# Kernel optimization log

Hardware: AMD Instinct MI355X
Metric: run time of the kernel (lower is better)

Reference implementation:

```python
import jax, jax.numpy as jnp
import numpy as np

NEG_SLOPE = 0.2  # PyG GATConv default negative_slope
N_NODES = 100000


def gat_conv(x, W, a_src, a_dst, src, dst, n_nodes):
    """One PyG-style GATConv (eval mode, self-loops already in src/dst).
    x: [N, in], W: [in, H*O], a_src/a_dst: [H, O]. Returns [N, H, O]."""
    heads, out_ch = a_src.shape
    h = (x @ W).reshape(n_nodes, heads, out_ch)          # [N,H,O]
    al_src = jnp.einsum('nho,ho->nh', h, a_src)          # [N,H]
    al_dst = jnp.einsum('nho,ho->nh', h, a_dst)          # [N,H]
    e = jax.nn.leaky_relu(al_src[src] + al_dst[dst], NEG_SLOPE)  # [E,H]
    # segment softmax over incoming edges of each dst node
    m = jax.ops.segment_max(e, dst, num_segments=n_nodes)       # [N,H]
    e = jnp.exp(e - m[dst])
    denom = jax.ops.segment_sum(e, dst, num_segments=n_nodes)   # [N,H]
    alpha = e / denom[dst]                                       # [E,H]
    msg = h[src] * alpha[:, :, None]                             # [E,H,O]
    return jax.ops.segment_sum(msg, dst, num_segments=n_nodes)  # [N,H,O]


def setup_inputs() -> dict:
    key = jax.random.key(0)
    ks = jax.random.split(key, 10)
    N, E = N_NODES, 3200000
    node_attr_dim, state_dim, heads, out_dim = 128, 8, 8, 1
    hid = state_dim * heads  # 64

    def glorot(k, shape, fan_in, fan_out):
        return jax.random.normal(k, shape, dtype=jnp.float32) * np.sqrt(2.0 / (fan_in + fan_out)).astype(np.float32)

    x = jax.random.normal(ks[0], (N, node_attr_dim), dtype=jnp.float32)
    edge_index = jax.random.randint(ks[1], (2, E), 0, N, dtype=jnp.int64)
    W1 = glorot(ks[2], (node_attr_dim, heads * state_dim), node_attr_dim, heads * state_dim)
    a_src1 = glorot(ks[3], (heads, state_dim), state_dim, 1)
    a_dst1 = glorot(ks[4], (heads, state_dim), state_dim, 1)
    b1 = jnp.zeros((hid,), dtype=jnp.float32)
    W2 = glorot(ks[5], (hid, out_dim), hid, out_dim)
    a_src2 = glorot(ks[6], (1, out_dim), out_dim, 1)
    a_dst2 = glorot(ks[7], (1, out_dim), out_dim, 1)
    b2 = jnp.zeros((out_dim,), dtype=jnp.float32)
    return {"x": x, "W1": W1, "a_src1": a_src1, "a_dst1": a_dst1, "b1": b1,
            "W2": W2, "a_src2": a_src2, "a_dst2": a_dst2, "b2": b2,
            "edge_index": edge_index}


def reference(x, W1, a_src1, a_dst1, b1, W2, a_src2, a_dst2, b2, edge_index):
    n = N_NODES
    loops = jnp.arange(n, dtype=edge_index.dtype)
    src = jnp.concatenate([edge_index[0], loops])  # add self-loops (PyG default)
    dst = jnp.concatenate([edge_index[1], loops])
    # layer 1: heads=8, concat -> [N, 64]
    h1 = gat_conv(x, W1, a_src1, a_dst1, src, dst, n)
    h1 = h1.reshape(n, -1) + b1
    h1 = jax.nn.relu(h1)  # dropout skipped (eval)
    # layer 2: heads=1, concat(size 1) -> [N, 1]
    h2 = gat_conv(h1, W2, a_src2, a_dst2, src, dst, n)
    out = h2.reshape(n, -1) + b2
    return out
```

## Files before the change

kernel.cpp:

```cpp
#include <hip/hip_runtime.h>
#include <math.h>

#define NEG 0.2f
#define CHUNK 16384

__device__ __forceinline__ float lrelu(float v) { return fmaxf(v, NEG * v); }

__device__ __forceinline__ unsigned short f2bf(float f) {
    unsigned u = __float_as_uint(f);
    u = (u + 0x7fffu + ((u >> 16) & 1u)) >> 16;
    return (unsigned short)u;
}
__device__ __forceinline__ float bf2f(unsigned short s) {
    return __uint_as_float((unsigned)s << 16);
}

__global__ __launch_bounds__(256) void k1(const float* __restrict__ x,
        const float* __restrict__ W1, const float* __restrict__ a_src,
        const float* __restrict__ a_dst,
        unsigned short* __restrict__ h1b, float* __restrict__ als,
        float* __restrict__ ald, int N)
{
    __shared__ float Wl[128 * 64];
    __shared__ float xt[128][68];

    const int tid = threadIdx.x;
    const int base = blockIdx.x * 64;

    const float4* Wv = (const float4*)W1;
    float4* Wlv = (float4*)Wl;
    for (int i = tid; i < 128 * 16; i += 256) Wlv[i] = Wv[i];

    for (int idx = tid; idx < 64 * 32; idx += 256) {
        int nl = idx >> 5;
        int k4 = (idx & 31) * 4;
        int n = base + nl;
        float4 v = make_float4(0.f, 0.f, 0.f, 0.f);
        if (n < N) v = *(const float4*)&x[(size_t)n * 128 + k4];
        xt[k4 + 0][nl] = v.x;
        xt[k4 + 1][nl] = v.y;
        xt[k4 + 2][nl] = v.z;
        xt[k4 + 3][nl] = v.w;
    }
    __syncthreads();

    const int wave = tid >> 6, lane = tid & 63;
    const int g = lane >> 4, c = lane & 15;
    const int nl0 = wave * 16 + 4 * g;

    float acc[4][4];
    #pragma unroll
    for (int j = 0; j < 4; ++j)
        #pragma unroll
        for (int t = 0; t < 4; ++t) acc[j][t] = 0.f;

    #pragma unroll 4
    for (int k = 0; k < 128; ++k) {
        float4 wv = *(const float4*)&Wl[k * 64 + 4 * c];
        float4 xv = *(const float4*)&xt[k][nl0];
        const float xs[4] = {xv.x, xv.y, xv.z, xv.w};
        const float wsv[4] = {wv.x, wv.y, wv.z, wv.w};
        #pragma unroll
        for (int j = 0; j < 4; ++j)
            #pragma unroll
            for (int t = 0; t < 4; ++t)
                acc[j][t] = fmaf(xs[j], wsv[t], acc[j][t]);
    }

    float a_s[4], a_d[4];
    #pragma unroll
    for (int t = 0; t < 4; ++t) { a_s[t] = a_src[4 * c + t]; a_d[t] = a_dst[4 * c + t]; }

    #pragma unroll
    for (int j = 0; j < 4; ++j) {
        int n = base + nl0 + j;
        float ps = 0.f, pd = 0.f;
        #pragma unroll
        for (int t = 0; t < 4; ++t) {
            ps = fmaf(acc[j][t], a_s[t], ps);
            pd = fmaf(acc[j][t], a_d[t], pd);
        }
        ps += __shfl_xor(ps, 1, 64);
        pd += __shfl_xor(pd, 1, 64);
        if (n < N) {
            ushort4 hb;
            hb.x = f2bf(acc[j][0]); hb.y = f2bf(acc[j][1]);
            hb.z = f2bf(acc[j][2]); hb.w = f2bf(acc[j][3]);
            *(ushort4*)&h1b[(size_t)n * 64 + 4 * c] = hb;
            if ((c & 1) == 0) {
                als[n * 8 + (c >> 1)] = ps;
                ald[n * 8 + (c >> 1)] = pd;
            }
        }
    }
}


__global__ __launch_bounds__(256) void p1(const int* __restrict__ ei, int E, int N,
        int* __restrict__ T, int NB, int NC)
{
    extern __shared__ int hist[];
    int tid = threadIdx.x;
    for (int b = tid; b < NB; b += 256) hist[b] = 0;
    __syncthreads();
    int base = blockIdx.x * CHUNK;
    for (int i = tid; i < CHUNK; i += 256) {
        int e = base + i;
        if (e >= E) break;
        int d = ei[E + e];
        if ((unsigned)d < (unsigned)N) atomicAdd(&hist[d >> 8], 1);
    }
    __syncthreads();
    for (int b = tid; b < NB; b += 256) T[b * NC + blockIdx.x] = hist[b];
}

__global__ __launch_bounds__(256) void p2a(int* __restrict__ T,
        int* __restrict__ total, int NB, int NC)
{
    int wave = threadIdx.x >> 6, lane = threadIdx.x & 63;
    int b = blockIdx.x * 4 + wave;
    if (b >= NB) return;
    int run = 0;
    for (int j0 = 0; j0 < NC; j0 += 64) {
        int j = j0 + lane;
        int orig = (j < NC) ? T[b * NC + j] : 0;
        int v = orig;
        #pragma unroll
        for (int off = 1; off < 64; off <<= 1) {
            int t = __shfl_up(v, off, 64);
            if (lane >= off) v += t;
        }
        if (j < NC) T[b * NC + j] = run + v - orig;
        run += __shfl(v, 63, 64);
    }
    if (lane == 0) total[b] = run;
}

__global__ __launch_bounds__(512) void p2b(const int* __restrict__ total,
        int* __restrict__ bstart, int nb)
{
    __shared__ int s[512];
    int tid = threadIdx.x;
    int run = 0;
    for (int base = 0; base < nb; base += 512) {
        int i = base + tid;
        int orig = (i < nb) ? total[i] : 0;
        s[tid] = orig;
        __syncthreads();
        #pragma unroll
        for (int off = 1; off < 512; off <<= 1) {
            int t = (tid >= off) ? s[tid - off] : 0;
            __syncthreads();
            s[tid] += t;
            __syncthreads();
        }
        if (i < nb) bstart[i] = run + s[tid] - orig;
        int tot = s[511];
        __syncthreads();
        run += tot;
    }
    if (tid == 0) bstart[nb] = run;
}

__global__ __launch_bounds__(256) void p3(const int* __restrict__ ei, int E, int N,
        const int* __restrict__ T, const int* __restrict__ bstart,
        unsigned* __restrict__ tmp, int NB, int NC)
{
    extern __shared__ int cur[];
    int tid = threadIdx.x;
    int j = blockIdx.x;
    for (int b = tid; b < NB; b += 256) cur[b] = bstart[b] + T[b * NC + j];
    __syncthreads();
    int base = j * CHUNK;
    for (int i = tid; i < CHUNK; i += 256) {
        int e = base + i;
        if (e >= E) break;
        int d = ei[E + e];
        if ((unsigned)d >= (unsigned)N) continue;
        int s = ei[e];
        if ((unsigned)s >= (unsigned)N) s = 0;
        int pos = atomicAdd(&cur[d >> 8], 1);
        if ((unsigned)pos < (unsigned)E)
            tmp[pos] = (unsigned)s | ((unsigned)(d & 255) << 24);
    }
}

__global__ __launch_bounds__(256) void p4(const unsigned* __restrict__ tmp,
        const int* __restrict__ bstart,
        int* __restrict__ cnt, int* __restrict__ rowptr, int* __restrict__ csr,
        int N, int E)
{
    __shared__ int hist[256];
    __shared__ int ssc[256];
    __shared__ int cur[256];
    int tid = threadIdx.x;
    int b = blockIdx.x;
    int s0 = bstart[b], s1 = bstart[b + 1];
    if (s0 < 0) s0 = 0; if (s0 > E) s0 = E;
    if (s1 < s0) s1 = s0; if (s1 > E) s1 = E;

    hist[tid] = 0;
    __syncthreads();
    for (int i = s0 + tid; i < s1; i += 256)
        atomicAdd(&hist[tmp[i] >> 24], 1);
    __syncthreads();

    int h = hist[tid];
    ssc[tid] = h;
    __syncthreads();
    #pragma unroll
    for (int off = 1; off < 256; off <<= 1) {
        int t = (tid >= off) ? ssc[tid - off] : 0;
        __syncthreads();
        ssc[tid] += t;
        __syncthreads();
    }
    int excl = ssc[tid] - h;
    int node = b * 256 + tid;
    if (node < N) {
        cnt[node] = h;
        rowptr[node] = s0 + excl;
    }
    cur[tid] = s0 + excl;
    __syncthreads();

    for (int i = s0 + tid; i < s1; i += 256) {
        unsigned v = tmp[i];
        int pos = atomicAdd(&cur[v >> 24], 1);
        if ((unsigned)pos < (unsigned)E) csr[pos] = (int)(v & 0xFFFFFFu);
    }
}


__global__ __launch_bounds__(256) void kh(const int* __restrict__ ei, int E, int N,
                                          int* __restrict__ cnt)
{
    int e = blockIdx.x * 256 + threadIdx.x;
    if (e >= E) return;
    int d = ei[E + e];
    if ((unsigned)d < (unsigned)N) atomicAdd(&cnt[d], 1);
}

__global__ __launch_bounds__(256) void ka(const int* __restrict__ cnt,
        int* __restrict__ rowptr, int* __restrict__ cursor,
        int* __restrict__ gtotal, int N)
{
    __shared__ int s[256];
    __shared__ int base;
    int tid = threadIdx.x;
    int g = blockIdx.x * 256 + tid;
    int v = (g < N) ? cnt[g] : 0;
    s[tid] = v;
    __syncthreads();
    #pragma unroll
    for (int off = 1; off < 256; off <<= 1) {
        int t = (tid >= off) ? s[tid - off] : 0;
        __syncthreads();
        s[tid] += t;
        __syncthreads();
    }
    if (tid == 255) base = atomicAdd(gtotal, s[255]);
    __syncthreads();
    if (g < N) {
        int r = base + s[tid] - v;
        rowptr[g] = r;
        cursor[g] = r;
    }
}

__global__ __launch_bounds__(256) void kc(const int* __restrict__ ei, int E, int N,
        int* __restrict__ cursor, int* __restrict__ csr)
{
    int e = blockIdx.x * 256 + threadIdx.x;
    if (e >= E) return;
    int s = ei[e];
    int d = ei[E + e];
    if ((unsigned)d >= (unsigned)N) return;
    int p = atomicAdd(&cursor[d], 1);
    if ((unsigned)p < (unsigned)E) csr[p] = s;
}

__global__ __launch_bounds__(256) void g1(const int* __restrict__ csr,
        const int* __restrict__ rowptr, const int* __restrict__ cnt,
        const unsigned short* __restrict__ h1b, const float* __restrict__ als,
        const float* __restrict__ ald,
        const float* __restrict__ b1, const float* __restrict__ W2,
        const float* __restrict__ a_src2, const float* __restrict__ a_dst2,
        float2* __restrict__ h2a, float* __restrict__ ald2, int N, int E)
{
    const int wave = threadIdx.x >> 6, lane = threadIdx.x & 63;
    const int n = blockIdx.x * 4 + wave;
    if (n >= N) return;

    const int s = lane >> 5;
    const int cp = lane & 31;
    const int hp = cp >> 2;

    const unsigned* h1w = (const unsigned*)h1b;

    const float ald_hp = ald[n * 8 + hp];
    float denp = 0.f;
    float acc0 = 0.f, acc1 = 0.f;

    int start = rowptr[n];
    int c = cnt[n];
    if ((unsigned)start >= (unsigned)E) { start = 0; c = 0; }
    if (c < 0) c = 0;
    if (start + c > E) c = E - start;

    for (int cbase = 0; cbase < c; cbase += 64) {
        int rem = c - cbase; if (rem > 64) rem = 64;
        int sv = 0;
        if (lane < rem) {
            int t = csr[start + cbase + lane];
            if ((unsigned)t < (unsigned)N) sv = t;
        }
        int steps = (rem + 1) >> 1;
        #pragma unroll 4
        for (int i = 0; i < steps; ++i) {
            int ge = 2 * i + s;
            int esrc = __shfl(sv, ge, 64);
            float w = __expf(lrelu(als[esrc * 8 + hp] + ald_hp));
            if (ge >= rem) w = 0.f;
            denp += w;
            unsigned u = h1w[(esrc << 5) + cp];
            acc0 = fmaf(w, __uint_as_float(u << 16), acc0);
            acc1 = fmaf(w, __uint_as_float(u & 0xffff0000u), acc1);
        }
    }

    float den = denp + __shfl_xor(denp, 32, 64);
    acc0 += __shfl_xor(acc0, 32, 64);
    acc1 += __shfl_xor(acc1, 32, 64);

    float wsf = __expf(lrelu(als[n * 8 + hp] + ald_hp));
    unsigned un = h1w[(n << 5) + cp];
    den += wsf;
    acc0 = fmaf(wsf, __uint_as_float(un << 16), acc0);
    acc1 = fmaf(wsf, __uint_as_float(un & 0xffff0000u), acc1);

    float2 bb = *(const float2*)&b1[2 * cp];
    float2 w2 = *(const float2*)&W2[2 * cp];
    float v0 = fmaxf(acc0 / den + bb.x, 0.f);
    float v1 = fmaxf(acc1 / den + bb.y, 0.f);
    float t = fmaf(v0, w2.x, v1 * w2.y);
    #pragma unroll
    for (int off = 1; off < 32; off <<= 1) t += __shfl_xor(t, off, 64);
    if (lane == 0) {
        float2 p;
        p.x = t;
        p.y = t * a_src2[0];
        h2a[n] = p;
        ald2[n] = t * a_dst2[0];
    }
}

__global__ __launch_bounds__(256) void g2(const int* __restrict__ csr,
        const int* __restrict__ rowptr, const int* __restrict__ cnt,
        const float2* __restrict__ h2a, const float* __restrict__ ald2,
        const float* __restrict__ b2, float* __restrict__ out, int N, int E)
{
    int sub = threadIdx.x >> 5;
    int l32 = threadIdx.x & 31;
    int n = blockIdx.x * 8 + sub;
    if (n >= N) return;

    float ad = ald2[n];
    int start = rowptr[n];
    int c = cnt[n];
    if ((unsigned)start >= (unsigned)E) { start = 0; c = 0; }
    if (c < 0) c = 0;
    if (start + c > E) c = E - start;

    float den = 0.f, acc = 0.f;
    for (int i = l32; i < c; i += 32) {
        int src = csr[start + i];
        if ((unsigned)src >= (unsigned)N) src = 0;
        float2 p = h2a[src];
        float w = __expf(lrelu(p.y + ad));
        den += w;
        acc = fmaf(w, p.x, acc);
    }
    #pragma unroll
    for (int off = 1; off < 32; off <<= 1) {
        den += __shfl_xor(den, off, 32);
        acc += __shfl_xor(acc, off, 32);
    }
    if (l32 == 0) {
        float2 p = h2a[n];
        float w0 = __expf(lrelu(p.y + ad));
        out[n] = (acc + w0 * p.x) / (den + w0) + b2[0];
    }
}

extern "C" void kernel_launch(void* const* d_in, const int* in_sizes, int n_in,
                              void* d_out, int out_size, void* d_ws, size_t ws_size,
                              hipStream_t stream)
{
    const float* x   = (const float*)d_in[0];
    const float* W1  = (const float*)d_in[1];
    const float* as1 = (const float*)d_in[2];
    const float* ad1 = (const float*)d_in[3];
    const float* b1  = (const float*)d_in[4];
    const float* W2  = (const float*)d_in[5];
    const float* as2 = (const float*)d_in[6];
    const float* ad2 = (const float*)d_in[7];
    const float* b2  = (const float*)d_in[8];
    const int*   ei  = (const int*)d_in[9];

    int N = in_sizes[0] / 128;
    int E = in_sizes[9] / 2;
    int NB = (N + 255) >> 8;
    int NC = (E + CHUNK - 1) / CHUNK;

    char* wsb = (char*)d_ws;
    size_t off = 0;
    auto alloc = [&](size_t bytes) -> char* {
        char* p = wsb + off;
        off = (off + bytes + 255) & ~(size_t)255;
        return p;
    };

    unsigned short* h1b = (unsigned short*)alloc((size_t)N * 64 * 2);
    float* als    = (float*)alloc((size_t)N * 8 * 4);
    float* ald    = (float*)alloc((size_t)N * 8 * 4);
    float2* h2a   = (float2*)alloc((size_t)N * 8);
    float* ald2   = (float*)alloc((size_t)N * 4);
    int* cnt      = (int*)alloc((size_t)N * 4);
    int* rowptr   = (int*)alloc((size_t)N * 4);
    int* csr      = (int*)alloc((size_t)E * 4);
    size_t common = off;

    int* T        = (int*)alloc((size_t)NB * NC * 4);
    int* total    = (int*)alloc((size_t)NB * 4);
    int* bstart   = (int*)alloc((size_t)(NB + 1) * 4);
    unsigned* tmp = (unsigned*)alloc((size_t)E * 4);
    size_t need_new = off;

    k1<<<(N + 63) / 64, 256, 0, stream>>>(x, W1, as1, ad1, h1b, als, ald, N);

    if (ws_size >= need_new && NB <= 512) {
        size_t lds = (size_t)NB * 4;
        p1<<<NC, 256, lds, stream>>>(ei, E, N, T, NB, NC);
        p2a<<<(NB + 3) / 4, 256, 0, stream>>>(T, total, NB, NC);
        p2b<<<1, 512, 0, stream>>>(total, bstart, NB);
        p3<<<NC, 256, lds, stream>>>(ei, E, N, T, bstart, tmp, NB, NC);
        p4<<<NB, 256, 0, stream>>>(tmp, bstart, cnt, rowptr, csr, N, E);
    } else {
        off = common;
        int* gtotal = (int*)alloc(32);
        int* cursor = (int*)alloc((size_t)N * 4);
        hipMemsetAsync(cnt, 0, (size_t)N * sizeof(int), stream);
        hipMemsetAsync(gtotal, 0, 32, stream);
        kh<<<(E + 255) / 256, 256, 0, stream>>>(ei, E, N, cnt);
        ka<<<(N + 255) / 256, 256, 0, stream>>>(cnt, rowptr, cursor, gtotal, N);
        kc<<<(E + 255) / 256, 256, 0, stream>>>(ei, E, N, cursor, csr);
    }

    g1<<<(N + 3) / 4, 256, 0, stream>>>(csr, rowptr, cnt, h1b, als, ald,
                                        b1, W2, as2, ad2, h2a, ald2, N, E);
    g2<<<(N + 7) / 8, 256, 0, stream>>>(csr, rowptr, cnt, h2a, ald2, b2,
                                        (float*)d_out, N, E);
}
```

Baseline: 416.3 us.

## Precompute per-edge attention weights once per lane and stage them in LDS

The layer-1 aggregation kernel previously had each of 32 channel lanes recompute exp(lrelu(...)) for every edge, with redundant scalar loads of als. Now each lane loads one edge's 8 head logits as two float4, computes all 8 weights once, accumulates the per-head denominators, and writes weights and source offsets to shared memory for the gather loop. This cuts redundant exp and attention loads. In exchange it adds block-wide __syncthreads per 64-edge chunk, which forces all four waves to iterate to the block's maximum degree, plus a 48-shuffle butterfly reduction for the denominators.

```diff
diff --git a/kernel.cpp b/kernel.cpp
--- a/kernel.cpp
+++ b/kernel.cpp
@@ -10,9 +10,6 @@
     unsigned u = __float_as_uint(f);
     u = (u + 0x7fffu + ((u >> 16) & 1u)) >> 16;
     return (unsigned short)u;
-}
-__device__ __forceinline__ float bf2f(unsigned short s) {
-    return __uint_as_float((unsigned)s << 16);
 }
 
 __global__ __launch_bounds__(256) void k1(const float* __restrict__ x,
@@ -288,53 +285,107 @@
         const float* __restrict__ a_src2, const float* __restrict__ a_dst2,
         float2* __restrict__ h2a, float* __restrict__ ald2, int N, int E)
 {
+    __shared__ float wl[4][8 * 65];
+    __shared__ int   sl[4][64];
+    __shared__ int   csh[4];
+
     const int wave = threadIdx.x >> 6, lane = threadIdx.x & 63;
     const int n = blockIdx.x * 4 + wave;
-    if (n >= N) return;
+    const bool active = (n < N);
+    const int n2 = active ? n : 0;
 
     const int s = lane >> 5;
     const int cp = lane & 31;
     const int hp = cp >> 2;
 
     const unsigned* h1w = (const unsigned*)h1b;
-
-    const float ald_hp = ald[n * 8 + hp];
-    float denp = 0.f;
+    const float4* als4 = (const float4*)als;
+    const float4* ald4 = (const float4*)ald;
+
+    float4 d0 = ald4[n2 * 2], d1 = ald4[n2 * 2 + 1];
+    float aldv[8] = {d0.x, d0.y, d0.z, d0.w, d1.x, d1.y, d1.z, d1.w};
+
+    float denv[8];
+    #pragma unroll
+    for (int i = 0; i < 8; ++i) denv[i] = 0.f;
     float acc0 = 0.f, acc1 = 0.f;
 
-    int start = rowptr[n];
-    int c = cnt[n];
+    int start = active ? rowptr[n2] : 0;
+    int c = active ? cnt[n2] : 0;
     if ((unsigned)start >= (unsigned)E) { start = 0; c = 0; }
     if (c < 0) c = 0;
     if (start + c > E) c = E - start;
 
-    for (int cbase = 0; cbase < c; cbase += 64) {
-        int rem = c - cbase; if (rem > 64) rem = 64;
-        int sv = 0;
+    if (lane == 0) csh[wave] = c;
+    __syncthreads();
+    int cmax = max(max(csh[0], csh[1]), max(csh[2], csh[3]));
+
+    float* wlw = wl[wave];
+    int* slw = sl[wave];
+
+    for (int cbase = 0; cbase < cmax; cbase += 64) {
+        int rem = c - cbase;
+        if (rem > 64) rem = 64;
+        if (rem < 0) rem = 0;
+
+        int esrc = 0;
         if (lane < rem) {
             int t = csr[start + cbase + lane];
-            if ((unsigned)t < (unsigned)N) sv = t;
-        }
+            if ((unsigned)t < (unsigned)N) esrc = t;
+        }
+        float4 a0 = als4[esrc * 2], a1 = als4[esrc * 2 + 1];
+        float wv[8];
+        wv[0] = __expf(lrelu(a0.x + aldv[0]));
+        wv[1] = __expf(lrelu(a0.y + aldv[1]));
+        wv[2] = __expf(lrelu(a0.z + aldv[2]));
+        wv[3] = __expf(lrelu(a0.w + aldv[3]));
+        wv[4] = __expf(lrelu(a1.x + aldv[4]));
+        wv[5] = __expf(lrelu(a1.y + aldv[5]));
+        wv[6] = __expf(lrelu(a1.z + aldv[6]));
+        wv[7] = __expf(lrelu(a1.w + aldv[7]));
+        if (lane >= rem) {
+            #pragma unroll
+            for (int i = 0; i < 8; ++i) wv[i] = 0.f;
+        }
+        #pragma unroll
+        for (int i = 0; i < 8; ++i) {
+            denv[i] += wv[i];
+            wlw[i * 65 + lane] = wv[i];
+        }
+        slw[lane] = esrc << 5;
+        __syncthreads();
+
         int steps = (rem + 1) >> 1;
         #pragma unroll 4
         for (int i = 0; i < steps; ++i) {
             int ge = 2 * i + s;
-            int esrc = __shfl(sv, ge, 64);
-            float w = __expf(lrelu(als[esrc * 8 + hp] + ald_hp));
-            if (ge >= rem) w = 0.f;
-            denp += w;
-            unsigned u = h1w[(esrc << 5) + cp];
+            float w = wlw[hp * 65 + ge];
+            int soff = slw[ge];
+            unsigned u = h1w[soff + cp];
             acc0 = fmaf(w, __uint_as_float(u << 16), acc0);
             acc1 = fmaf(w, __uint_as_float(u & 0xffff0000u), acc1);
         }
-    }
-
-    float den = denp + __shfl_xor(denp, 32, 64);
+        __syncthreads();
+    }
+
+    #pragma unroll
+    for (int off = 1; off < 64; off <<= 1) {
+        #pragma unroll
+        for (int i = 0; i < 8; ++i) denv[i] += __shfl_xor(denv[i], off, 64);
+    }
+    float q0 = (hp & 1) ? denv[1] : denv[0];
+    float q1 = (hp & 1) ? denv[3] : denv[2];
+    float q2 = (hp & 1) ? denv[5] : denv[4];
+    float q3 = (hp & 1) ? denv[7] : denv[6];
+    float r0 = (hp & 2) ? q1 : q0;
+    float r1 = (hp & 2) ? q3 : q2;
+    float den = (hp & 4) ? r1 : r0;
+
     acc0 += __shfl_xor(acc0, 32, 64);
     acc1 += __shfl_xor(acc1, 32, 64);
 
-    float wsf = __expf(lrelu(als[n * 8 + hp] + ald_hp));
-    unsigned un = h1w[(n << 5) + cp];
+    float wsf = __expf(lrelu(als[n2 * 8 + hp] + aldv[hp]));
+    unsigned un = h1w[(n2 << 5) + cp];
     den += wsf;
     acc0 = fmaf(wsf, __uint_as_float(un << 16), acc0);
     acc1 = fmaf(wsf, __uint_as_float(un & 0xffff0000u), acc1);
@@ -346,7 +397,7 @@
     float t = fmaf(v0, w2.x, v1 * w2.y);
     #pragma unroll
     for (int off = 1; off < 32; off <<= 1) t += __shfl_xor(t, off, 64);
-    if (lane == 0) {
+    if (active && lane == 0) {
         float2 p;
         p.x = t;
         p.y = t * a_src2[0];
```

Result: faster. 387.3 us (-7.0%).
